# Kernel tuning notes

Measured on AMD Instinct MI355X. Metric: run time of the kernel, lower is better.

## Reference

```python
import jax, jax.numpy as jnp
import numpy as np

EPS = 1e-5
NUM_HEAD = 8
D_MODEL = 512
D_K = D_MODEL // NUM_HEAD
SCALE = np.float32(1.0 / np.sqrt(D_K))


def _ln(x, g, b):
    m = jnp.mean(x, axis=-1, keepdims=True)
    v = jnp.var(x, axis=-1, keepdims=True)
    return g * (x - m) * jax.lax.rsqrt(v + EPS) + b


def setup_inputs() -> dict:
    key = jax.random.key(0)
    ks = jax.random.split(key, 24)
    B, W, S, V, D = 16, 256, 16, 32, D_MODEL
    DF = 2 * D
    w = lambda k, shape: (jax.random.normal(k, shape, jnp.float32) * 0.02)
    inp = {
        "text": jax.random.normal(ks[0], (B, W, D), jnp.float32),
        "av_feat": jax.random.normal(ks[1], (B, S, V, D), jnp.float32),
        "text_mask": jnp.ones((B, W, W), dtype=bool),
        "attn_sent_index": jnp.sort(jax.random.randint(ks[2], (B, W), 0, S), axis=-1),
        # res1 LayerNorm
        "ln_res1_g": jnp.ones((D,), jnp.float32), "ln_res1_b": jnp.zeros((D,), jnp.float32),
        # self-attention projections
        "sa_wq": w(ks[3], (D, D)), "sa_bq": jnp.zeros((D,), jnp.float32),
        "sa_wk": w(ks[4], (D, D)), "sa_bk": jnp.zeros((D,), jnp.float32),
        "sa_wv": w(ks[5], (D, D)), "sa_bv": jnp.zeros((D,), jnp.float32),
        "sa_wo": w(ks[6], (D, D)), "sa_bo": jnp.zeros((D,), jnp.float32),
        # cross-attention norms + projections
        "ca_ln_text_g": jnp.ones((D,), jnp.float32), "ca_ln_text_b": jnp.zeros((D,), jnp.float32),
        "ca_ln_av_g": jnp.ones((D,), jnp.float32), "ca_ln_av_b": jnp.zeros((D,), jnp.float32),
        "ca_wq": w(ks[7], (D, D)), "ca_bq": jnp.zeros((D,), jnp.float32),
        "ca_wk": w(ks[8], (D, D)), "ca_bk": jnp.zeros((D,), jnp.float32),
        "ca_wv": w(ks[9], (D, D)), "ca_bv": jnp.zeros((D,), jnp.float32),
        # post-cross norms
        "ln1_g": jnp.ones((D,), jnp.float32), "ln1_b": jnp.zeros((D,), jnp.float32),
        "ln2_g": jnp.ones((D,), jnp.float32), "ln2_b": jnp.zeros((D,), jnp.float32),
        # res2 LayerNorm + FFN (d_ff = 2*d_model per source)
        "ln_res2_g": jnp.ones((D,), jnp.float32), "ln_res2_b": jnp.zeros((D,), jnp.float32),
        "ff_w1": w(ks[10], (D, DF)), "ff_b1": jnp.zeros((DF,), jnp.float32),
        "ff_w2": w(ks[11], (DF, D)), "ff_b2": jnp.zeros((D,), jnp.float32),
    }
    return inp


def reference(text, av_feat, text_mask, attn_sent_index,
              ln_res1_g, ln_res1_b,
              sa_wq, sa_bq, sa_wk, sa_bk, sa_wv, sa_bv, sa_wo, sa_bo,
              ca_ln_text_g, ca_ln_text_b, ca_ln_av_g, ca_ln_av_b,
              ca_wq, ca_bq, ca_wk, ca_bk, ca_wv, ca_bv,
              ln1_g, ln1_b, ln2_g, ln2_b,
              ln_res2_g, ln_res2_b, ff_w1, ff_b1, ff_w2, ff_b2):
    B, W, D = text.shape
    S, V = av_feat.shape[1], av_feat.shape[2]

    # ---- res1: x + self_attn(norm(x)) (dropout = identity in eval) ----
    x = _ln(text, ln_res1_g, ln_res1_b)
    q = (x @ sa_wq + sa_bq).reshape(B, W, NUM_HEAD, D_K)
    k = (x @ sa_wk + sa_bk).reshape(B, W, NUM_HEAD, D_K)
    v = (x @ sa_wv + sa_bv).reshape(B, W, NUM_HEAD, D_K)
    scores = jnp.einsum('bqhd,bkhd->bhqk', q, k) * SCALE
    scores = jnp.where(text_mask[:, None, :, :], scores, jnp.float32(-1e9))
    a = jax.nn.softmax(scores, axis=-1)
    sa = jnp.einsum('bhqk,bkhd->bqhd', a, v).reshape(B, W, D) @ sa_wo + sa_bo
    text = text + sa

    # ---- cross attention: index-gathered sigmoid attention ----
    tn = _ln(text, ca_ln_text_g, ca_ln_text_b)
    an = _ln(av_feat, ca_ln_av_g, ca_ln_av_b)
    cq = (tn @ ca_wq + ca_bq).reshape(B, W, 1, NUM_HEAD, D_K)
    ck = (an @ ca_wk + ca_bk).reshape(B, S, V, NUM_HEAD, D_K)
    cv = (an @ ca_wv + ca_bv).reshape(B, S, V, NUM_HEAD, D_K)
    bidx = jnp.arange(B)[:, None]
    ck = ck[bidx, attn_sent_index]  # [B, W, V, H, Dk]
    cv = cv[bidx, attn_sent_index]  # [B, W, V, H, Dk]
    att = jax.nn.sigmoid(jnp.sum(cq * ck, axis=-1, keepdims=True) * SCALE)  # [B,W,V,H,1]
    res = jnp.sum(att * cv, axis=-3).reshape(B, W, D)

    text = _ln(text, ln1_g, ln1_b) + _ln(res, ln2_g, ln2_b)  # av_weight = 1

    # ---- res2: x + FFN(norm(x)) ----
    y = _ln(text, ln_res2_g, ln_res2_b)
    text = text + (jax.nn.relu(y @ ff_w1 + ff_b1) @ ff_w2 + ff_b2)

    attn_out = jnp.mean(att, axis=-2)[..., 0]  # mean over heads -> [B, W, V]
    return (text, attn_out)
```

## Files before the change

kernel.cpp:

```cpp
#include <hip/hip_runtime.h>
#include <hip/hip_bf16.h>


#define D_MODEL 512
#define NUM_HEAD 8
#define SCALE 0.125f
#define EPS 1e-5f

typedef __hip_bfloat16 bf16;
typedef __attribute__((ext_vector_type(8))) short short8;
typedef __attribute__((ext_vector_type(4))) float floatx4;

static __device__ __forceinline__ float s2f(short u) {
    unsigned int x = ((unsigned int)(unsigned short)u) << 16;
    float f; __builtin_memcpy(&f, &x, 4); return f;
}
static __device__ __forceinline__ short f2s(float f) {
    bf16 t = __float2bfloat16(f);
    short s; __builtin_memcpy(&s, &t, 2); return s;
}

struct TransArgs {
    const float* src[9];
    bf16* dst[9];
    int K[9], N[9];
    int start[10];
};

__global__ __launch_bounds__(256) void transpose_kernel(TransArgs a) {
    int bid = blockIdx.x;
    int m = 0;
    while (bid >= a.start[m + 1]) m++;
    const int t = bid - a.start[m];
    const int N = a.N[m], K = a.K[m];
    const int tilesX = N >> 5;
    const int tx = t % tilesX, ty = t / tilesX;
    __shared__ bf16 tile[32][33];
    const int tid = threadIdx.x;
    const int r = tid >> 3, c0 = (tid & 7) * 4;
    const float* sp = a.src[m] + (size_t)(ty * 32 + r) * N + tx * 32 + c0;
    float4 v = *(const float4*)sp;
    tile[r][c0 + 0] = __float2bfloat16(v.x);
    tile[r][c0 + 1] = __float2bfloat16(v.y);
    tile[r][c0 + 2] = __float2bfloat16(v.z);
    tile[r][c0 + 3] = __float2bfloat16(v.w);
    __syncthreads();
    bf16* dp = a.dst[m] + (size_t)(tx * 32 + r) * K + ty * 32 + c0;
    #pragma unroll
    for (int i = 0; i < 4; i++) dp[i] = tile[c0 + i][r];
}

static __device__ __forceinline__ void ln_body(const float* __restrict__ inp,
                                               const float* __restrict__ g,
                                               const float* __restrict__ bta,
                                               bf16* __restrict__ out,
                                               size_t row, int t) {
    const float x0 = inp[row * D_MODEL + t];
    const float x1 = inp[row * D_MODEL + t + 256];
    float s = x0 + x1, sq = x0 * x0 + x1 * x1;
    #pragma unroll
    for (int off = 32; off >= 1; off >>= 1) {
        s += __shfl_xor(s, off, 64);
        sq += __shfl_xor(sq, off, 64);
    }
    __shared__ float ws_[4], wq_[4];
    if ((t & 63) == 0) { ws_[t >> 6] = s; wq_[t >> 6] = sq; }
    __syncthreads();
    s = ws_[0] + ws_[1] + ws_[2] + ws_[3];
    sq = wq_[0] + wq_[1] + wq_[2] + wq_[3];
    const float m = s * (1.f / D_MODEL);
    const float var = sq * (1.f / D_MODEL) - m * m;
    const float r = rsqrtf(var + EPS);
    out[row * D_MODEL + t]       = __float2bfloat16(g[t]       * (x0 - m) * r + bta[t]);
    out[row * D_MODEL + t + 256] = __float2bfloat16(g[t + 256] * (x1 - m) * r + bta[t + 256]);
}

__global__ __launch_bounds__(256) void ln_kernel(const float* __restrict__ inp,
                                                 const float* __restrict__ g,
                                                 const float* __restrict__ bta,
                                                 bf16* __restrict__ out) {
    ln_body(inp, g, bta, out, blockIdx.x, threadIdx.x);
}

__global__ __launch_bounds__(256) void ln_dual_kernel(const float* __restrict__ inA,
                                                      const float* __restrict__ gA,
                                                      const float* __restrict__ bA,
                                                      bf16* __restrict__ outA, int nA,
                                                      const float* __restrict__ inB,
                                                      const float* __restrict__ gB,
                                                      const float* __restrict__ bB,
                                                      bf16* __restrict__ outB) {
    const int r = blockIdx.x;
    if (r < nA) ln_body(inA, gA, bA, outA, r, threadIdx.x);
    else        ln_body(inB, gB, bB, outB, r - nA, threadIdx.x);
}

__global__ __launch_bounds__(256) void ln2_add_ln_kernel(const float* __restrict__ a,
                                                         const float* __restrict__ c,
                                                         const float* __restrict__ g1,
                                                         const float* __restrict__ b1,
                                                         const float* __restrict__ g2,
                                                         const float* __restrict__ b2,
                                                         const float* __restrict__ g3,
                                                         const float* __restrict__ b3,
                                                         float* __restrict__ text2,
                                                         bf16* __restrict__ y) {
    const size_t row = blockIdx.x;
    const int t = threadIdx.x;
    const float a0 = a[row * D_MODEL + t], a1 = a[row * D_MODEL + t + 256];
    const float c0 = c[row * D_MODEL + t], c1 = c[row * D_MODEL + t + 256];
    float sa = a0 + a1, qa = a0 * a0 + a1 * a1;
    float sc = c0 + c1, qc = c0 * c0 + c1 * c1;
    #pragma unroll
    for (int off = 32; off >= 1; off >>= 1) {
        sa += __shfl_xor(sa, off, 64); qa += __shfl_xor(qa, off, 64);
        sc += __shfl_xor(sc, off, 64); qc += __shfl_xor(qc, off, 64);
    }
    __shared__ float r_[4][4];
    if ((t & 63) == 0) { int w = t >> 6; r_[0][w] = sa; r_[1][w] = qa; r_[2][w] = sc; r_[3][w] = qc; }
    __syncthreads();
    sa = r_[0][0] + r_[0][1] + r_[0][2] + r_[0][3];
    qa = r_[1][0] + r_[1][1] + r_[1][2] + r_[1][3];
    sc = r_[2][0] + r_[2][1] + r_[2][2] + r_[2][3];
    qc = r_[3][0] + r_[3][1] + r_[3][2] + r_[3][3];
    const float ma = sa * (1.f / D_MODEL), mc = sc * (1.f / D_MODEL);
    const float ra = rsqrtf(qa * (1.f / D_MODEL) - ma * ma + EPS);
    const float rc = rsqrtf(qc * (1.f / D_MODEL) - mc * mc + EPS);
    const float v0 = g1[t] * (a0 - ma) * ra + b1[t] + g2[t] * (c0 - mc) * rc + b2[t];
    const float v1 = g1[t + 256] * (a1 - ma) * ra + b1[t + 256]
                   + g2[t + 256] * (c1 - mc) * rc + b2[t + 256];
    text2[row * D_MODEL + t] = v0;
    text2[row * D_MODEL + t + 256] = v1;
    float sv = v0 + v1, qv = v0 * v0 + v1 * v1;
    #pragma unroll
    for (int off = 32; off >= 1; off >>= 1) {
        sv += __shfl_xor(sv, off, 64); qv += __shfl_xor(qv, off, 64);
    }
    __syncthreads();
    if ((t & 63) == 0) { int w = t >> 6; r_[0][w] = sv; r_[1][w] = qv; }
    __syncthreads();
    sv = r_[0][0] + r_[0][1] + r_[0][2] + r_[0][3];
    qv = r_[1][0] + r_[1][1] + r_[1][2] + r_[1][3];
    const float mv = sv * (1.f / D_MODEL);
    const float rv = rsqrtf(qv * (1.f / D_MODEL) - mv * mv + EPS);
    y[row * D_MODEL + t]       = __float2bfloat16(g3[t]       * (v0 - mv) * rv + b3[t]);
    y[row * D_MODEL + t + 256] = __float2bfloat16(g3[t + 256] * (v1 - mv) * rv + b3[t + 256]);
}

template <int RES, bool RELU, bool OUT_BF16>
__global__ __launch_bounds__(256) void gemm2(const bf16* __restrict__ A,
                                             const bf16* __restrict__ BT,
                                             const float* __restrict__ bias,
                                             const float* __restrict__ resid,
                                             void* __restrict__ C,
                                             int M, int N, int K) {
    __shared__ short As[128 * 72];
    __shared__ short Bs[64 * 72];
    const int tid = threadIdx.x;
    const int lane = tid & 63, w = tid >> 6;
    const int quad = lane >> 4, l15 = lane & 15;
    const int wm = (w >> 1) * 64, wn = (w & 1) * 32;
    const int m0 = blockIdx.y * 128, n0 = blockIdx.x * 64;
    const short* Ag = (const short*)A;
    const short* Bg = (const short*)BT;
    floatx4 acc[4][2] = {};
    for (int kk0 = 0; kk0 < K; kk0 += 64) {
        #pragma unroll
        for (int p = 0; p < 4; p++) {
            const int e = p * 2048 + tid * 8;
            const int row = e >> 6, col = e & 63;
            *(short8*)&As[row * 72 + col] = *(const short8*)&Ag[(size_t)(m0 + row) * K + kk0 + col];
        }
        #pragma unroll
        for (int p = 0; p < 2; p++) {
            const int e = p * 2048 + tid * 8;
            const int row = e >> 6, col = e & 63;
            *(short8*)&Bs[row * 72 + col] = *(const short8*)&Bg[(size_t)(n0 + row) * K + kk0 + col];
        }
        __syncthreads();
        #pragma unroll
        for (int ks = 0; ks < 2; ks++) {
            const int kc = ks * 32 + quad * 8;
            short8 b0 = *(const short8*)&Bs[(wn + l15) * 72 + kc];
            short8 b1 = *(const short8*)&Bs[(wn + 16 + l15) * 72 + kc];
            #pragma unroll
            for (int mi = 0; mi < 4; mi++) {
                short8 am = *(const short8*)&As[(wm + mi * 16 + l15) * 72 + kc];
                acc[mi][0] = __builtin_amdgcn_mfma_f32_16x16x32_bf16(am, b0, acc[mi][0], 0, 0, 0);
                acc[mi][1] = __builtin_amdgcn_mfma_f32_16x16x32_bf16(am, b1, acc[mi][1], 0, 0, 0);
            }
        }
        __syncthreads();
    }
    #pragma unroll
    for (int mi = 0; mi < 4; mi++)
        #pragma unroll
        for (int ni = 0; ni < 2; ni++)
            #pragma unroll
            for (int r = 0; r < 4; r++) {
                const int row = m0 + wm + mi * 16 + quad * 4 + r;
                const int col = n0 + wn + ni * 16 + l15;
                float v = acc[mi][ni][r] + bias[col];
                if (RELU) v = fmaxf(v, 0.f);
                if (RES == 1) v += resid[(size_t)row * N + col];
                if (OUT_BF16) ((bf16*)C)[(size_t)row * N + col] = __float2bfloat16(v);
                else          ((float*)C)[(size_t)row * N + col] = v;
            }
}

__global__ __launch_bounds__(256) void gemm_fused(const bf16* __restrict__ A,
                                                  const bf16* __restrict__ BT,
                                                  const float* __restrict__ b0p,
                                                  const float* __restrict__ b1p,
                                                  const float* __restrict__ b2p,
                                                  bf16* __restrict__ C,
                                                  int M, int Ntot, int K) {
    __shared__ short As[128 * 72];
    __shared__ short Bs[64 * 72];
    const int tid = threadIdx.x;
    const int lane = tid & 63, w = tid >> 6;
    const int quad = lane >> 4, l15 = lane & 15;
    const int wm = (w >> 1) * 64, wn = (w & 1) * 32;
    const int m0 = blockIdx.y * 128, n0 = blockIdx.x * 64;
    const int seg = n0 >> 9;
    const float* bias = (seg == 0) ? b0p : ((seg == 1) ? b1p : b2p);
    const short* Ag = (const short*)A;
    const short* Bg = (const short*)BT;
    floatx4 acc[4][2] = {};
    for (int kk0 = 0; kk0 < K; kk0 += 64) {
        #pragma unroll
        for (int p = 0; p < 4; p++) {
            const int e = p * 2048 + tid * 8;
            const int row = e >> 6, col = e & 63;
            *(short8*)&As[row * 72 + col] = *(const short8*)&Ag[(size_t)(m0 + row) * K + kk0 + col];
        }
        #pragma unroll
        for (int p = 0; p < 2; p++) {
            const int e = p * 2048 + tid * 8;
            const int row = e >> 6, col = e & 63;
            *(short8*)&Bs[row * 72 + col] = *(const short8*)&Bg[(size_t)(n0 + row) * K + kk0 + col];
        }
        __syncthreads();
        #pragma unroll
        for (int ks = 0; ks < 2; ks++) {
            const int kc = ks * 32 + quad * 8;
            short8 b0 = *(const short8*)&Bs[(wn + l15) * 72 + kc];
            short8 b1 = *(const short8*)&Bs[(wn + 16 + l15) * 72 + kc];
            #pragma unroll
            for (int mi = 0; mi < 4; mi++) {
                short8 am = *(const short8*)&As[(wm + mi * 16 + l15) * 72 + kc];
                acc[mi][0] = __builtin_amdgcn_mfma_f32_16x16x32_bf16(am, b0, acc[mi][0], 0, 0, 0);
                acc[mi][1] = __builtin_amdgcn_mfma_f32_16x16x32_bf16(am, b1, acc[mi][1], 0, 0, 0);
            }
        }
        __syncthreads();
    }
    #pragma unroll
    for (int mi = 0; mi < 4; mi++)
        #pragma unroll
        for (int ni = 0; ni < 2; ni++)
            #pragma unroll
            for (int r = 0; r < 4; r++) {
                const int row = m0 + wm + mi * 16 + quad * 4 + r;
                const int col = n0 + wn + ni * 16 + l15;
                C[(size_t)row * Ntot + col] = __float2bfloat16(acc[mi][ni][r] + bias[col & 511]);
            }
}

__global__ __launch_bounds__(256) void self_attn_mfma(const bf16* __restrict__ q,
                                                      const bf16* __restrict__ k,
                                                      const bf16* __restrict__ v,
                                                      int ld,
                                                      bf16* __restrict__ sa) {
    const int qc = blockIdx.x, h = blockIdx.y, b = blockIdx.z;
    const int tid = threadIdx.x, lane = tid & 63, w = tid >> 6;
    const int quad = lane >> 4, l15 = lane & 15;
    __shared__ short Kt[64 * 72];
    __shared__ short VT[64 * 72];
    __shared__ short Ps[4][16 * 72];
    const int qrow = b * 256 + qc * 64 + w * 16 + l15;
    const short* qg = (const short*)q + (size_t)qrow * ld + h * 64;
    short8 qf0 = *(const short8*)&qg[quad * 8];
    short8 qf1 = *(const short8*)&qg[32 + quad * 8];
    floatx4 o[4] = {};
    float den[4] = {};
    for (int kt0 = 0; kt0 < 256; kt0 += 64) {
        __syncthreads();
        {
            const int row = tid >> 2, c0 = (tid & 3) * 16;
            const short* kg = (const short*)k + (size_t)(b * 256 + kt0 + row) * ld + h * 64 + c0;
            *(short8*)&Kt[row * 72 + c0]     = *(const short8*)kg;
            *(short8*)&Kt[row * 72 + c0 + 8] = *(const short8*)(kg + 8);
        }
        {
            const int key = tid & 63, dk0 = (tid >> 6) * 16;
            const short* vg = (const short*)v + (size_t)(b * 256 + kt0 + key) * ld + h * 64 + dk0;
            short8 v0 = *(const short8*)vg;
            short8 v1 = *(const short8*)(vg + 8);
            #pragma unroll
            for (int i = 0; i < 8; i++) VT[(dk0 + i) * 72 + key] = v0[i];
            #pragma unroll
            for (int i = 0; i < 8; i++) VT[(dk0 + 8 + i) * 72 + key] = v1[i];
        }
        __syncthreads();
        floatx4 sacc[4] = {};
        #pragma unroll
        for (int ni = 0; ni < 4; ni++) {
            short8 b0 = *(const short8*)&Kt[(ni * 16 + l15) * 72 + quad * 8];
            short8 b1 = *(const short8*)&Kt[(ni * 16 + l15) * 72 + 32 + quad * 8];
            sacc[ni] = __builtin_amdgcn_mfma_f32_16x16x32_bf16(qf0, b0, sacc[ni], 0, 0, 0);
            sacc[ni] = __builtin_amdgcn_mfma_f32_16x16x32_bf16(qf1, b1, sacc[ni], 0, 0, 0);
        }
        #pragma unroll
        for (int ni = 0; ni < 4; ni++)
            #pragma unroll
            for (int r = 0; r < 4; r++) {
                const float e = __expf(sacc[ni][r] * SCALE);
                den[r] += e;
                Ps[w][(quad * 4 + r) * 72 + ni * 16 + l15] = f2s(e);
            }
        #pragma unroll
        for (int kc = 0; kc < 2; kc++) {
            short8 af = *(const short8*)&Ps[w][l15 * 72 + kc * 32 + quad * 8];
            #pragma unroll
            for (int ni = 0; ni < 4; ni++) {
                short8 bv = *(const short8*)&VT[(ni * 16 + l15) * 72 + kc * 32 + quad * 8];
                o[ni] = __builtin_amdgcn_mfma_f32_16x16x32_bf16(af, bv, o[ni], 0, 0, 0);
            }
        }
    }
    #pragma unroll
    for (int off = 1; off < 16; off <<= 1)
        #pragma unroll
        for (int r = 0; r < 4; r++) den[r] += __shfl_xor(den[r], off, 64);
    float inv[4];
    #pragma unroll
    for (int r = 0; r < 4; r++) inv[r] = 1.f / den[r];
    const int qo = b * 256 + qc * 64 + w * 16 + quad * 4;
    #pragma unroll
    for (int ni = 0; ni < 4; ni++)
        #pragma unroll
        for (int r = 0; r < 4; r++)
            sa[(size_t)(qo + r) * D_MODEL + h * 64 + ni * 16 + l15] =
                __float2bfloat16(o[ni][r] * inv[r]);
}

__global__ __launch_bounds__(256) void cross_attn3(const bf16* __restrict__ kv,
                                                   const bf16* __restrict__ cq,
                                                   const int* __restrict__ sidx,
                                                   float* __restrict__ res,
                                                   float* __restrict__ out_attn) {
    const int s = blockIdx.x, b = blockIdx.y, t = threadIdx.x;
    __shared__ int wrange[2];
    __shared__ short Ks[32 * 576];
    __shared__ short Vs[32 * 576];
    __shared__ short qs[32 * 576];
    __shared__ float att[32 * 256];
    if (t == 0) { wrange[0] = 256; wrange[1] = 0; }
    __syncthreads();
    const int* sb = sidx + b * 256;
    {
        const int sv = sb[t];
        if (sv == s) {
            if (t == 0 || sb[t - 1] != s) wrange[0] = t;
            if (t == 255 || sb[t + 1] != s) wrange[1] = t + 1;
        }
    }
    {
        const int v = t >> 3, hh = t & 7;
        const short* kg = (const short*)kv + ((size_t)((b * 16 + s) * 32 + v)) * 1024 + hh * 64;
        const short* vg = kg + 512;
        short* kd = &Ks[v * 576 + hh * 72];
        short* vd = &Vs[v * 576 + hh * 72];
        #pragma unroll
        for (int c = 0; c < 8; c++) {
            *(short8*)&kd[c * 8] = *(const short8*)&kg[c * 8];
            *(short8*)&vd[c * 8] = *(const short8*)&vg[c * 8];
        }
    }
    __syncthreads();
    const int w0 = wrange[0], w1 = wrange[1];
    const int h2 = t >> 5, dp = t & 31;
    const short* cqg = (const short*)cq;
    for (int wc = w0; wc < w1; wc += 32) {
        const int len = (w1 - wc < 32) ? (w1 - wc) : 32;
        for (int i = t; i < len * 64; i += 256) {
            const int e = i * 8;
            const int row = e >> 9, col = e & 511;
            *(short8*)&qs[row * 576 + (col >> 6) * 72 + (col & 63)] =
                *(const short8*)&cqg[((size_t)(b * 256 + wc + row)) * 512 + col];
        }
        __syncthreads();
        for (int i = t; i < len * 256; i += 256) {
            const int wl = i >> 8, r = i & 255, v = r >> 3, h = r & 7;
            const short* qp = &qs[wl * 576 + h * 72];
            const short* kp = &Ks[v * 576 + h * 72];
            float dot = 0.f;
            #pragma unroll
            for (int c = 0; c < 8; c++) {
                short8 q8 = *(const short8*)&qp[c * 8];
                short8 k8 = *(const short8*)&kp[c * 8];
                dot += s2f(q8[0]) * s2f(k8[0]) + s2f(q8[1]) * s2f(k8[1])
                     + s2f(q8[2]) * s2f(k8[2]) + s2f(q8[3]) * s2f(k8[3])
                     + s2f(q8[4]) * s2f(k8[4]) + s2f(q8[5]) * s2f(k8[5])
                     + s2f(q8[6]) * s2f(k8[6]) + s2f(q8[7]) * s2f(k8[7]);
            }
            att[wl * 256 + r] = 1.f / (1.f + __expf(-dot * SCALE));
        }
        __syncthreads();
        for (int wl = 0; wl < len; wl++) {
            float r0 = 0.f, r1 = 0.f;
            #pragma unroll
            for (int vv = 0; vv < 32; ++vv) {
                const float av = att[wl * 256 + vv * 8 + h2];
                const int pv = *(const int*)&Vs[vv * 576 + h2 * 72 + dp * 2];
                r0 += av * s2f((short)(pv & 0xffff));
                r1 += av * s2f((short)(pv >> 16));
            }
            *(float2*)&res[((size_t)(b * 256 + wc + wl)) * 512 + h2 * 64 + dp * 2] =
                make_float2(r0, r1);
        }
        if (t < 32) {
            for (int wl = 0; wl < len; wl++) {
                float m = 0.f;
                #pragma unroll
                for (int j = 0; j < 8; j++) m += att[wl * 256 + t * 8 + j];
                out_attn[((size_t)(b * 256 + wc + wl)) * 32 + t] = m * 0.125f;
            }
        }
        __syncthreads();
    }
}

extern "C" void kernel_launch(void* const* d_in, const int* in_sizes, int n_in,
                              void* d_out, int out_size, void* d_ws, size_t ws_size,
                              hipStream_t stream) {
    const int B = 16, S = 16;
    const int M1 = 4096, M2 = 8192;

    const float* text = (const float*)d_in[0];
    const float* av   = (const float*)d_in[1];
    const int* sidx   = (const int*)d_in[3];
    const float* ln_res1_g = (const float*)d_in[4];
    const float* ln_res1_b = (const float*)d_in[5];
    const float* sa_wq = (const float*)d_in[6];
    const float* sa_bq = (const float*)d_in[7];
    const float* sa_wk = (const float*)d_in[8];
    const float* sa_bk = (const float*)d_in[9];
    const float* sa_wv = (const float*)d_in[10];
    const float* sa_bv = (const float*)d_in[11];
    const float* sa_wo = (const float*)d_in[12];
    const float* sa_bo = (const float*)d_in[13];
    const float* ca_ln_text_g = (const float*)d_in[14];
    const float* ca_ln_text_b = (const float*)d_in[15];
    const float* ca_ln_av_g = (const float*)d_in[16];
    const float* ca_ln_av_b = (const float*)d_in[17];
    const float* ca_wq = (const float*)d_in[18];
    const float* ca_bq = (const float*)d_in[19];
    const float* ca_wk = (const float*)d_in[20];
    const float* ca_bk = (const float*)d_in[21];
    const float* ca_wv = (const float*)d_in[22];
    const float* ca_bv = (const float*)d_in[23];
    const float* ln1_g = (const float*)d_in[24];
    const float* ln1_b = (const float*)d_in[25];
    const float* ln2_g = (const float*)d_in[26];
    const float* ln2_b = (const float*)d_in[27];
    const float* ln_res2_g = (const float*)d_in[28];
    const float* ln_res2_b = (const float*)d_in[29];
    const float* ff_w1 = (const float*)d_in[30];
    const float* ff_b1 = (const float*)d_in[31];
    const float* ff_w2 = (const float*)d_in[32];
    const float* ff_b2 = (const float*)d_in[33];

    char* wsb = (char*)d_ws;
    const size_t MBy = 1024 * 1024;
    bf16*  WT    = (bf16*)(wsb);
    bf16*  xln   = (bf16*)(wsb + 6 * MBy);
    bf16*  qkv   = (bf16*)(wsb + 10 * MBy);
    bf16*  sab   = (bf16*)(wsb + 22 * MBy);
    float* text1 = (float*)(wsb + 26 * MBy);
    bf16*  tn    = (bf16*)(wsb + 34 * MBy);
    bf16*  an    = (bf16*)(wsb + 38 * MBy);
    bf16*  cqb   = (bf16*)(wsb + 46 * MBy);
    bf16*  kvb   = (bf16*)(wsb + 50 * MBy);
    float* res   = (float*)(wsb + 66 * MBy);
    float* text2 = (float*)(wsb + 74 * MBy);
    bf16*  y     = (bf16*)(wsb + 82 * MBy);
    bf16*  h1    = (bf16*)(wsb + 86 * MBy);

    bf16* wqT  = WT;
    bf16* cwqT = WT + 1048576;
    bf16* cwkT = WT + 1310720;
    bf16* woT  = WT + 786432;
    bf16* f1T  = WT + 1835008;
    bf16* f2T  = WT + 2359296;

    float* out_text = (float*)d_out;
    float* out_attn = (float*)d_out + (size_t)M1 * D_MODEL;

    TransArgs ta;
    const float* srcs[9] = {sa_wq, sa_wk, sa_wv, sa_wo, ca_wq, ca_wk, ca_wv, ff_w1, ff_w2};
    bf16* dsts[9] = {wqT, WT + 262144, WT + 524288, woT, cwqT, cwkT, WT + 1572864, f1T, f2T};
    const int Ks_[9] = {512, 512, 512, 512, 512, 512, 512, 512, 1024};
    const int Ns_[9] = {512, 512, 512, 512, 512, 512, 512, 1024, 512};
    int cum = 0;
    for (int i = 0; i < 9; i++) {
        ta.src[i] = srcs[i]; ta.dst[i] = dsts[i]; ta.K[i] = Ks_[i]; ta.N[i] = Ns_[i];
        ta.start[i] = cum;
        cum += (Ks_[i] >> 5) * (Ns_[i] >> 5);
    }
    ta.start[9] = cum;
    transpose_kernel<<<cum, 256, 0, stream>>>(ta);

    const dim3 blk256(256);
    const dim3 gD(8, 32);
    const dim3 gQKV(24, 32);
    const dim3 gKV(16, 64);
    const dim3 gF1(16, 32);

    ln_kernel<<<M1, blk256, 0, stream>>>(text, ln_res1_g, ln_res1_b, xln);
    gemm_fused<<<gQKV, blk256, 0, stream>>>(xln, wqT, sa_bq, sa_bk, sa_bv, qkv, M1, 1536, D_MODEL);
    self_attn_mfma<<<dim3(4, NUM_HEAD, B), blk256, 0, stream>>>(qkv, qkv + 512, qkv + 1024, 1536, sab);
    gemm2<1, false, false><<<gD, blk256, 0, stream>>>(sab, woT, sa_bo, text, text1, M1, D_MODEL, D_MODEL);
    ln_dual_kernel<<<M1 + M2, blk256, 0, stream>>>(text1, ca_ln_text_g, ca_ln_text_b, tn, M1,
                                                   av, ca_ln_av_g, ca_ln_av_b, an);
    gemm2<0, false, true><<<gD, blk256, 0, stream>>>(tn, cwqT, ca_bq, nullptr, cqb, M1, D_MODEL, D_MODEL);
    gemm_fused<<<gKV, blk256, 0, stream>>>(an, cwkT, ca_bk, ca_bv, ca_bv, kvb, M2, 1024, D_MODEL);
    cross_attn3<<<dim3(S, B), blk256, 0, stream>>>(kvb, cqb, sidx, res, out_attn);
    ln2_add_ln_kernel<<<M1, blk256, 0, stream>>>(text1, res, ln1_g, ln1_b, ln2_g, ln2_b,
                                                 ln_res2_g, ln_res2_b, text2, y);
    gemm2<0, true, true><<<gF1, blk256, 0, stream>>>(y, f1T, ff_b1, nullptr, h1, M1, 1024, D_MODEL);
    gemm2<1, false, false><<<gD, blk256, 0, stream>>>(h1, f2T, ff_b2, text2, out_text, M1, D_MODEL, 1024);
}
```

Baseline: 287.9 us.

## Merge weight transpose with input LayerNorms and batch QKV and cross-KV GEMMs

```diff
diff --git a/kernel.cpp b/kernel.cpp
--- a/kernel.cpp
+++ b/kernel.cpp
@@ -27,8 +27,54 @@
     int start[10];
 };
 
-__global__ __launch_bounds__(256) void transpose_kernel(TransArgs a) {
-    int bid = blockIdx.x;
+static __device__ __forceinline__ void ln_body(const float* __restrict__ inp,
+                                               const float* __restrict__ g,
+                                               const float* __restrict__ bta,
+                                               bf16* __restrict__ out,
+                                               size_t row, int t) {
+    const float x0 = inp[row * D_MODEL + t];
+    const float x1 = inp[row * D_MODEL + t + 256];
+    float s = x0 + x1, sq = x0 * x0 + x1 * x1;
+    #pragma unroll
+    for (int off = 32; off >= 1; off >>= 1) {
+        s += __shfl_xor(s, off, 64);
+        sq += __shfl_xor(sq, off, 64);
+    }
+    __shared__ float ws_[4], wq_[4];
+    if ((t & 63) == 0) { ws_[t >> 6] = s; wq_[t >> 6] = sq; }
+    __syncthreads();
+    s = ws_[0] + ws_[1] + ws_[2] + ws_[3];
+    sq = wq_[0] + wq_[1] + wq_[2] + wq_[3];
+    const float m = s * (1.f / D_MODEL);
+    const float var = sq * (1.f / D_MODEL) - m * m;
+    const float r = rsqrtf(var + EPS);
+    out[row * D_MODEL + t]       = __float2bfloat16(g[t]       * (x0 - m) * r + bta[t]);
+    out[row * D_MODEL + t + 256] = __float2bfloat16(g[t + 256] * (x1 - m) * r + bta[t + 256]);
+}
+
+__global__ __launch_bounds__(256) void ln_kernel(const float* __restrict__ inp,
+                                                 const float* __restrict__ g,
+                                                 const float* __restrict__ bta,
+                                                 bf16* __restrict__ out) {
+    ln_body(inp, g, bta, out, blockIdx.x, threadIdx.x);
+}
+
+__global__ __launch_bounds__(256) void prologue_kernel(TransArgs a, int nT,
+                                                       const float* __restrict__ text,
+                                                       const float* __restrict__ g1,
+                                                       const float* __restrict__ b1,
+                                                       bf16* __restrict__ xln,
+                                                       const float* __restrict__ av,
+                                                       const float* __restrict__ g2,
+                                                       const float* __restrict__ b2,
+                                                       bf16* __restrict__ an) {
+    const int bid = blockIdx.x;
+    if (bid >= nT) {
+        const int r = bid - nT;
+        if (r < 4096) ln_body(text, g1, b1, xln, r, threadIdx.x);
+        else          ln_body(av, g2, b2, an, r - 4096, threadIdx.x);
+        return;
+    }
     int m = 0;
     while (bid >= a.start[m + 1]) m++;
     const int t = bid - a.start[m];
@@ -48,51 +94,6 @@
     bf16* dp = a.dst[m] + (size_t)(tx * 32 + r) * K + ty * 32 + c0;
     #pragma unroll
     for (int i = 0; i < 4; i++) dp[i] = tile[c0 + i][r];
-}
-
-static __device__ __forceinline__ void ln_body(const float* __restrict__ inp,
-                                               const float* __restrict__ g,
-                                               const float* __restrict__ bta,
-                                               bf16* __restrict__ out,
-                                               size_t row, int t) {
-    const float x0 = inp[row * D_MODEL + t];
-    const float x1 = inp[row * D_MODEL + t + 256];
-    float s = x0 + x1, sq = x0 * x0 + x1 * x1;
-    #pragma unroll
-    for (int off = 32; off >= 1; off >>= 1) {
-        s += __shfl_xor(s, off, 64);
-        sq += __shfl_xor(sq, off, 64);
-    }
-    __shared__ float ws_[4], wq_[4];
-    if ((t & 63) == 0) { ws_[t >> 6] = s; wq_[t >> 6] = sq; }
-    __syncthreads();
-    s = ws_[0] + ws_[1] + ws_[2] + ws_[3];
-    sq = wq_[0] + wq_[1] + wq_[2] + wq_[3];
-    const float m = s * (1.f / D_MODEL);
-    const float var = sq * (1.f / D_MODEL) - m * m;
-    const float r = rsqrtf(var + EPS);
-    out[row * D_MODEL + t]       = __float2bfloat16(g[t]       * (x0 - m) * r + bta[t]);
-    out[row * D_MODEL + t + 256] = __float2bfloat16(g[t + 256] * (x1 - m) * r + bta[t + 256]);
-}
-
-__global__ __launch_bounds__(256) void ln_kernel(const float* __restrict__ inp,
-                                                 const float* __restrict__ g,
-                                                 const float* __restrict__ bta,
-                                                 bf16* __restrict__ out) {
-    ln_body(inp, g, bta, out, blockIdx.x, threadIdx.x);
-}
-
-__global__ __launch_bounds__(256) void ln_dual_kernel(const float* __restrict__ inA,
-                                                      const float* __restrict__ gA,
-                                                      const float* __restrict__ bA,
-                                                      bf16* __restrict__ outA, int nA,
-                                                      const float* __restrict__ inB,
-                                                      const float* __restrict__ gB,
-                                                      const float* __restrict__ bB,
-                                                      bf16* __restrict__ outB) {
-    const int r = blockIdx.x;
-    if (r < nA) ln_body(inA, gA, bA, outA, r, threadIdx.x);
-    else        ln_body(inB, gB, bB, outB, r - nA, threadIdx.x);
 }
 
 __global__ __launch_bounds__(256) void ln2_add_ln_kernel(const float* __restrict__ a,
@@ -208,20 +209,18 @@
             }
 }
 
-__global__ __launch_bounds__(256) void gemm_fused(const bf16* __restrict__ A,
-                                                  const bf16* __restrict__ BT,
-                                                  const float* __restrict__ b0p,
-                                                  const float* __restrict__ b1p,
-                                                  const float* __restrict__ b2p,
-                                                  bf16* __restrict__ C,
-                                                  int M, int Ntot, int K) {
-    __shared__ short As[128 * 72];
-    __shared__ short Bs[64 * 72];
+static __device__ __forceinline__ void gemm_fused_body(const bf16* __restrict__ A,
+                                                       const bf16* __restrict__ BT,
+                                                       const float* __restrict__ b0p,
+                                                       const float* __restrict__ b1p,
+                                                       const float* __restrict__ b2p,
+                                                       bf16* __restrict__ C,
+                                                       int Ntot, int K, int m0, int n0,
+                                                       short* As, short* Bs) {
     const int tid = threadIdx.x;
     const int lane = tid & 63, w = tid >> 6;
     const int quad = lane >> 4, l15 = lane & 15;
     const int wm = (w >> 1) * 64, wn = (w & 1) * 32;
-    const int m0 = blockIdx.y * 128, n0 = blockIdx.x * 64;
     const int seg = n0 >> 9;
     const float* bias = (seg == 0) ? b0p : ((seg == 1) ? b1p : b2p);
     const short* Ag = (const short*)A;
@@ -265,6 +264,30 @@
                 const int col = n0 + wn + ni * 16 + l15;
                 C[(size_t)row * Ntot + col] = __float2bfloat16(acc[mi][ni][r] + bias[col & 511]);
             }
+}
+
+__global__ __launch_bounds__(256) void gemm_qkv_kv(const bf16* __restrict__ xln,
+                                                   const bf16* __restrict__ wqT,
+                                                   const float* __restrict__ bq,
+                                                   const float* __restrict__ bk,
+                                                   const float* __restrict__ bv,
+                                                   bf16* __restrict__ qkv,
+                                                   const bf16* __restrict__ an,
+                                                   const bf16* __restrict__ cwkT,
+                                                   const float* __restrict__ cbk,
+                                                   const float* __restrict__ cbv,
+                                                   bf16* __restrict__ kvb) {
+    __shared__ short As[128 * 72];
+    __shared__ short Bs[64 * 72];
+    const int bid = blockIdx.x;
+    if (bid < 768) {
+        gemm_fused_body(xln, wqT, bq, bk, bv, qkv, 1536, 512,
+                        (bid / 24) * 128, (bid % 24) * 64, As, Bs);
+    } else {
+        const int r = bid - 768;
+        gemm_fused_body(an, cwkT, cbk, cbv, cbv, kvb, 1024, 512,
+                        (r / 16) * 128, (r % 16) * 64, As, Bs);
+    }
 }
 
 __global__ __launch_bounds__(256) void self_attn_mfma(const bf16* __restrict__ q,
@@ -510,22 +533,20 @@
         cum += (Ks_[i] >> 5) * (Ns_[i] >> 5);
     }
     ta.start[9] = cum;
-    transpose_kernel<<<cum, 256, 0, stream>>>(ta);
 
     const dim3 blk256(256);
     const dim3 gD(8, 32);
-    const dim3 gQKV(24, 32);
-    const dim3 gKV(16, 64);
     const dim3 gF1(16, 32);
 
-    ln_kernel<<<M1, blk256, 0, stream>>>(text, ln_res1_g, ln_res1_b, xln);
-    gemm_fused<<<gQKV, blk256, 0, stream>>>(xln, wqT, sa_bq, sa_bk, sa_bv, qkv, M1, 1536, D_MODEL);
+    prologue_kernel<<<cum + M1 + M2, blk256, 0, stream>>>(ta, cum,
+                                                          text, ln_res1_g, ln_res1_b, xln,
+                                                          av, ca_ln_av_g, ca_ln_av_b, an);
+    gemm_qkv_kv<<<1792, blk256, 0, stream>>>(xln, wqT, sa_bq, sa_bk, sa_bv, qkv,
+                                             an, cwkT, ca_bk, ca_bv, kvb);
     self_attn_mfma<<<dim3(4, NUM_HEAD, B), blk256, 0, stream>>>(qkv, qkv + 512, qkv + 1024, 1536, sab);
     gemm2<1, false, false><<<gD, blk256, 0, stream>>>(sab, woT, sa_bo, text, text1, M1, D_MODEL, D_MODEL);
-    ln_dual_kernel<<<M1 + M2, blk256, 0, stream>>>(text1, ca_ln_text_g, ca_ln_text_b, tn, M1,
-                                                   av, ca_ln_av_g, ca_ln_av_b, an);
+    ln_kernel<<<M1, blk256, 0, stream>>>(text1, ca_ln_text_g, ca_ln_text_b, tn);
     gemm2<0, false, true><<<gD, blk256, 0, stream>>>(tn, cwqT, ca_bq, nullptr, cqb, M1, D_MODEL, D_MODEL);
-    gemm_fused<<<gKV, blk256, 0, stream>>>(an, cwkT, ca_bk, ca_bv, ca_bv, kvb, M2, 1024, D_MODEL);
     cross_attn3<<<dim3(S, B), blk256, 0, stream>>>(kvb, cqb, sidx, res, out_attn);
     ln2_add_ln_kernel<<<M1, blk256, 0, stream>>>(text1, res, ln1_g, ln1_b, ln2_g, ln2_b,
                                                  ln_res2_g, ln_res2_b, text2, y);
```

Measured after the change: 278.5 us. 3.3% less time.
